# Optimization experiments

Hardware: AMD Instinct MI355X
Metric: run time of the kernel (lower is better)

## Reference

```python
import jax, jax.numpy as jnp
import numpy as np

B, C, T = 8, 256, 2048
DS = 4
SC = C // DS          # tsa_scale = 64
DEPTH = 256           # temporal_depth (band width)
BN_EPS = 1e-5


def _conv_bn_relu(x, W, b, g, beta, mu, var):
    # 1x1 conv on [B, C, T, 1] layout == channel matmul, then eval-mode BN, then ReLU
    y = jnp.einsum('bctz,oc->botz', x, W) + b[None, :, None, None]
    inv = g / jnp.sqrt(var + BN_EPS)
    y = (y - mu[None, :, None, None]) * inv[None, :, None, None] + beta[None, :, None, None]
    return jax.nn.relu(y)


def setup_inputs() -> dict:
    key = jax.random.key(0)
    ks = jax.random.split(key, 20)
    inp = {"x": jax.random.normal(ks[0], (B, C, T, 1), jnp.float32)}
    for name, oc, base in (("k", SC, 1), ("q", SC, 7), ("v", C, 13)):
        inp[name + "W"] = jax.random.normal(ks[base], (oc, C), jnp.float32) * 0.05
        inp[name + "b"] = jax.random.normal(ks[base + 1], (oc,), jnp.float32) * 0.05
        inp[name + "g"] = 1.0 + 0.05 * jax.random.normal(ks[base + 2], (oc,), jnp.float32)
        inp[name + "beta"] = jax.random.normal(ks[base + 3], (oc,), jnp.float32) * 0.05
        inp[name + "mu"] = jax.random.normal(ks[base + 4], (oc,), jnp.float32) * 0.05
        inp[name + "var"] = 1.0 + 0.1 * jax.random.uniform(ks[base + 5], (oc,), jnp.float32)
    return inp


def reference(x, kW, kb, kg, kbeta, kmu, kvar,
              qW, qb, qg, qbeta, qmu, qvar,
              vW, vb, vg, vbeta, vmu, vvar):
    key = _conv_bn_relu(x, kW, kb, kg, kbeta, kmu, kvar)[..., 0]                      # [B, SC, T]
    query = _conv_bn_relu(x, qW, qb, qg, qbeta, qmu, qvar)[..., 0].transpose(0, 2, 1)  # [B, T, SC]
    value = _conv_bn_relu(x, vW, vb, vg, vbeta, vmu, vvar)[..., 0].transpose(0, 2, 1)  # [B, T, C]

    i = jnp.arange(T)
    # tril(diag=0) * triu(diag=-(DEPTH-1)): causal band of width DEPTH
    mask = ((i[:, None] >= i[None, :]) & (i[:, None] - i[None, :] <= DEPTH - 1)).astype(x.dtype)

    s = jnp.einsum('btd,bds->bts', query, key) * mask / np.float32(np.sqrt(SC))
    s = jnp.exp(s - jnp.max(s, axis=2, keepdims=True)) * mask
    # NOTE: original torch code does `torch.sum(...)[0]`, indexing batch 0 of the
    # sum tensor ([T,1]) and broadcasting it across the batch. Replicated faithfully.
    s = s / (jnp.sum(s, axis=2, keepdims=True)[0] + 1e-30)

    tsa_out = jnp.einsum('bts,bsc->btc', s, value)                                     # [B, T, C]
    return x + tsa_out.transpose(0, 2, 1)[..., None]                                   # res_skip
```

## Files before the change

### kernel.cpp

```cpp
#include <hip/hip_runtime.h>

#define TDIM 2048

typedef __bf16 bf16_t;
typedef bf16_t bf16x8 __attribute__((ext_vector_type(8)));
typedef float f32x4 __attribute__((ext_vector_type(4)));
typedef unsigned short us8 __attribute__((ext_vector_type(8)));

__device__ __forceinline__ unsigned short f2bf(float x) {
  unsigned u = __builtin_bit_cast(unsigned, x);
  u += 0x7fffu + ((u >> 16) & 1u);
  return (unsigned short)(u >> 16);
}

__device__ __forceinline__ void gl_lds16(const unsigned short* g, unsigned short* l) {
  __builtin_amdgcn_global_load_lds(
      (const __attribute__((address_space(1))) unsigned int*)g,
      (__attribute__((address_space(3))) unsigned int*)l, 16, 0, 0);
}

__global__ __launch_bounds__(256) void k_prepw(
    const float* __restrict__ kW, const float* __restrict__ kb,
    const float* __restrict__ kg, const float* __restrict__ kbe,
    const float* __restrict__ kmu, const float* __restrict__ kva,
    const float* __restrict__ qW, const float* __restrict__ qb,
    const float* __restrict__ qg, const float* __restrict__ qbe,
    const float* __restrict__ qmu, const float* __restrict__ qva,
    const float* __restrict__ vW, const float* __restrict__ vb,
    const float* __restrict__ vg, const float* __restrict__ vbe,
    const float* __restrict__ vmu, const float* __restrict__ vva,
    unsigned short* __restrict__ effWf,
    float* __restrict__ effb)
{
  const int idx = blockIdx.x;
  const int tid = threadIdx.x;
  const int gid = idx >> 2, cc = idx & 3;
  unsigned short* dst = effWf + (size_t)idx * 8192;
#pragma unroll
  for (int pass = 0; pass < 4; ++pass) {
    int f = pass * 256 + tid;
    int ocblk = f >> 7, cblk = (f >> 4) & 7, m = f & 15;
    int G = gid * 128 + ocblk * 16 + m;
    const float* Wp = (G < 64) ? (kW + G * 256)
                     : (G < 128) ? (qW + (G - 64) * 256)
                                 : (vW + (G - 128) * 256);
    float gg = (G < 64) ? kg[G]  : (G < 128) ? qg[G - 64]  : vg[G - 128];
    float vr = (G < 64) ? kva[G] : (G < 128) ? qva[G - 64] : vva[G - 128];
    float inv = gg * rsqrtf(vr + 1e-5f);
    int c = cc * 64 + cblk * 8;
    float4 a = *(const float4*)(Wp + c);
    float4 bq = *(const float4*)(Wp + c + 4);
    ushort4 lo, hi;
    lo.x = f2bf(a.x * inv);  lo.y = f2bf(a.y * inv);
    lo.z = f2bf(a.z * inv);  lo.w = f2bf(a.w * inv);
    hi.x = f2bf(bq.x * inv); hi.y = f2bf(bq.y * inv);
    hi.z = f2bf(bq.z * inv); hi.w = f2bf(bq.w * inv);
    *(ushort4*)(dst + f * 8) = lo;
    *(ushort4*)(dst + f * 8 + 4) = hi;
  }
  if (idx == 0) {
    for (int G = tid; G < 384; G += 256) {
      float gg = (G < 64) ? kg[G]  : (G < 128) ? qg[G - 64]  : vg[G - 128];
      float vr = (G < 64) ? kva[G] : (G < 128) ? qva[G - 64] : vva[G - 128];
      float bb = (G < 64) ? kb[G]  : (G < 128) ? qb[G - 64]  : vb[G - 128];
      float mm = (G < 64) ? kmu[G] : (G < 128) ? qmu[G - 64] : vmu[G - 128];
      float be = (G < 64) ? kbe[G] : (G < 128) ? qbe[G - 64] : vbe[G - 128];
      float inv = gg * rsqrtf(vr + 1e-5f);
      effb[G] = (bb - mm) * inv + be;
    }
  }
}

__global__ __launch_bounds__(256, 3) void k_qkv(
    const unsigned short* __restrict__ effWf,
    const float* __restrict__ effb,
    const float* __restrict__ x,
    unsigned short* __restrict__ vv,
    unsigned short* __restrict__ kTs,
    unsigned short* __restrict__ qTs)
{
  const int tb = blockIdx.x, gid = blockIdx.y, b = blockIdx.z;
  const int tid = threadIdx.x;
  const int lane = tid & 63, wv = tid >> 6;
  const int m = lane & 15, quad = lane >> 4;
  const int t0 = tb * 64;

  __shared__ unsigned short Wb[2][8192];
  __shared__ unsigned short Xs[4608];
  __shared__ float effbs[128];

  if (tid < 128) effbs[tid] = effb[gid * 128 + tid];

  const unsigned short* wbase = effWf + (size_t)gid * 32768;
  const float* xb = x + (size_t)b * 256 * TDIM + t0 + lane;

  float xr[16];

  auto stageW = [&](int cc, int bufi) {
    const unsigned short* ws = wbase + cc * 8192;
#pragma unroll
    for (int i = 0; i < 4; ++i) {
      int ii = wv * 4 + i;
      gl_lds16(ws + (ii * 64 + lane) * 8, &Wb[bufi][ii * 512]);
    }
  };
  auto loadX = [&](int cc) {
#pragma unroll
    for (int p = 0; p < 4; ++p)
#pragma unroll
      for (int j = 0; j < 4; ++j) {
        int c = cc * 64 + p * 16 + wv * 4 + j;
        xr[p * 4 + j] = xb[(size_t)c * TDIM];
      }
  };

  const f32x4 fz = {0.f, 0.f, 0.f, 0.f};
  f32x4 acc[2][4];
#pragma unroll
  for (int i = 0; i < 2; ++i)
#pragma unroll
    for (int j = 0; j < 4; ++j) acc[i][j] = fz;

  stageW(0, 0);
  loadX(0);
  for (int cc = 0; cc < 4; ++cc) {
    __syncthreads();
#pragma unroll
    for (int p = 0; p < 4; ++p) {
      int cb4 = p * 16 + wv * 4;
      int swz = (((cb4 >> 3) ^ (lane >> 3)) << 3) | (cb4 & 7);
      ushort4 s4;
      s4.x = f2bf(xr[p * 4 + 0]); s4.y = f2bf(xr[p * 4 + 1]);
      s4.z = f2bf(xr[p * 4 + 2]); s4.w = f2bf(xr[p * 4 + 3]);
      *(ushort4*)&Xs[lane * 72 + swz] = s4;
    }
    if (cc < 3) { stageW(cc + 1, (cc + 1) & 1); loadX(cc + 1); }
    __syncthreads();
    const unsigned short* Wc = Wb[cc & 1];
#pragma unroll
    for (int kk = 0; kk < 2; ++kk) {
      int cb = kk * 4 + quad;
      bf16x8 af[2], bfv[4];
#pragma unroll
      for (int mt = 0; mt < 2; ++mt)
        af[mt] = *(const bf16x8*)&Wc[(((wv * 2 + mt) * 8 + cb) * 16 + m) * 8];
#pragma unroll
      for (int nt = 0; nt < 4; ++nt) {
        int t = nt * 16 + m;
        bfv[nt] = *(const bf16x8*)&Xs[t * 72 + ((cb ^ (t >> 3)) << 3)];
      }
#pragma unroll
      for (int mt = 0; mt < 2; ++mt)
#pragma unroll
        for (int nt = 0; nt < 4; ++nt)
          acc[mt][nt] = __builtin_amdgcn_mfma_f32_16x16x32_bf16(af[mt], bfv[nt], acc[mt][nt], 0, 0, 0);
    }
  }

  if (gid == 0) {
#pragma unroll
    for (int mt = 0; mt < 2; ++mt)
#pragma unroll
      for (int nt = 0; nt < 4; ++nt) {
        int ocl = wv * 32 + mt * 16 + quad * 4;
        int t = t0 + nt * 16 + m;
        ushort4 s4;
        s4.x = f2bf(fmaxf(acc[mt][nt][0] + effbs[ocl + 0], 0.f));
        s4.y = f2bf(fmaxf(acc[mt][nt][1] + effbs[ocl + 1], 0.f));
        s4.z = f2bf(fmaxf(acc[mt][nt][2] + effbs[ocl + 2], 0.f));
        s4.w = f2bf(fmaxf(acc[mt][nt][3] + effbs[ocl + 3], 0.f));
        if (ocl < 64) {
          int col = (((ocl >> 3) ^ (t & 7)) << 3) | (ocl & 7);
          *(ushort4*)(kTs + ((size_t)(b * TDIM + t)) * 64 + col) = s4;
        } else {
          int oq = ocl - 64;
          int col = (((oq >> 3) ^ (t & 7)) << 3) | (oq & 7);
          *(ushort4*)(qTs + ((size_t)(b * TDIM + t)) * 64 + col) = s4;
        }
      }
  } else {
#pragma unroll
    for (int mt = 0; mt < 2; ++mt)
#pragma unroll
      for (int nt = 0; nt < 4; ++nt)
#pragma unroll
        for (int r = 0; r < 4; ++r) {
          int ocl = wv * 32 + mt * 16 + quad * 4 + r;
          float y = fmaxf(acc[mt][nt][r] + effbs[ocl], 0.f);
          int c = (gid - 1) * 128 + ocl;
          int t = t0 + nt * 16 + m;
          vv[(size_t)(b * 256 + c) * TDIM + t] = f2bf(y);
        }
  }
}

__global__ __launch_bounds__(512, 1) void k_denom(
    const unsigned short* __restrict__ kTs,
    const unsigned short* __restrict__ qTs,
    float* __restrict__ denom0)
{
  const int t0d = blockIdx.x * 16;
  const int tid = threadIdx.x;
  const int lane = tid & 63, w = tid >> 6;
  const int m = lane & 15, quad = lane >> 4;

  __shared__ unsigned short S[18432];
  unsigned short* Qs = S;
  unsigned short* Ks = S + 1024;
  __shared__ float pmaxs[8][16];
  __shared__ float psums[8][16];

  {
    const unsigned short* qg = qTs + (size_t)t0d * 64;
    const unsigned short* kg = kTs + ((long)t0d - 256) * 64;
#pragma unroll
    for (int it = 0; it < 5; ++it) {
      int j = it * 512 + tid;
      if (j < 2304) {
        const unsigned short* g = (j < 128) ? (qg + j * 8) : (kg + (size_t)(j - 128) * 8);
        gl_lds16(g, &S[(it * 512 + w * 64) * 8]);
      }
    }
  }
  __syncthreads();

  const int jn = (w == 0) ? 3 : 2;
  f32x4 sc[3];
  {
    int t = m;
    bf16x8 qf0 = *(const bf16x8*)&Qs[t * 64 + ((quad ^ (t & 7)) << 3)];
    bf16x8 qf1 = *(const bf16x8*)&Qs[t * 64 + (((4 + quad) ^ (t & 7)) << 3)];
    const f32x4 fz = {0.f, 0.f, 0.f, 0.f};
#pragma unroll
    for (int jj = 0; jj < 3; ++jj) {
      if (jj < jn) {
        int j = w + jj * 8;
        int sr = 16 * j + m;
        f32x4 a = fz;
        bf16x8 kf0 = *(const bf16x8*)&Ks[sr * 64 + ((quad ^ (sr & 7)) << 3)];
        a = __builtin_amdgcn_mfma_f32_16x16x32_bf16(qf0, kf0, a, 0, 0, 0);
        bf16x8 kf1 = *(const bf16x8*)&Ks[sr * 64 + (((4 + quad) ^ (sr & 7)) << 3)];
        a = __builtin_amdgcn_mfma_f32_16x16x32_bf16(qf1, kf1, a, 0, 0, 0);
        sc[jj] = a;
      }
    }
  }

  float mx[4] = {0.f, 0.f, 0.f, 0.f};
#pragma unroll
  for (int jj = 0; jj < 3; ++jj)
    if (jj < jn) {
      int j = w + jj * 8;
#pragma unroll
      for (int r = 0; r < 4; ++r) {
        float v = sc[jj][r] * 0.125f;
        sc[jj][r] = v;
        int tg = t0d + quad * 4 + r;
        int sg = t0d - 256 + 16 * j + m;
        if (sg >= 0 && sg <= tg && tg - sg < 256) mx[r] = fmaxf(mx[r], v);
      }
    }
#pragma unroll
  for (int d = 1; d < 16; d <<= 1)
#pragma unroll
    for (int r = 0; r < 4; ++r) mx[r] = fmaxf(mx[r], __shfl_xor(mx[r], d, 64));
  if (m == 0)
#pragma unroll
    for (int r = 0; r < 4; ++r) pmaxs[w][quad * 4 + r] = mx[r];
  __syncthreads();

  float mxf[4];
#pragma unroll
  for (int r = 0; r < 4; ++r) {
    float v = pmaxs[0][quad * 4 + r];
#pragma unroll
    for (int ww = 1; ww < 8; ++ww) v = fmaxf(v, pmaxs[ww][quad * 4 + r]);
    mxf[r] = v;
  }
  float sm[4] = {0.f, 0.f, 0.f, 0.f};
#pragma unroll
  for (int jj = 0; jj < 3; ++jj)
    if (jj < jn) {
      int j = w + jj * 8;
#pragma unroll
      for (int r = 0; r < 4; ++r) {
        int tg = t0d + quad * 4 + r;
        int sg = t0d - 256 + 16 * j + m;
        if (sg >= 0 && sg <= tg && tg - sg < 256) sm[r] += __expf(sc[jj][r] - mxf[r]);
      }
    }
#pragma unroll
  for (int d = 1; d < 16; d <<= 1)
#pragma unroll
    for (int r = 0; r < 4; ++r) sm[r] += __shfl_xor(sm[r], d, 64);
  if (m == 0)
#pragma unroll
    for (int r = 0; r < 4; ++r) psums[w][quad * 4 + r] = sm[r];
  __syncthreads();

  if (tid < 16) {
    float s = 0.f;
#pragma unroll
    for (int ww = 0; ww < 8; ++ww) s += psums[ww][tid];
    denom0[t0d + tid] = s;
  }
}

__global__ __launch_bounds__(512, 4) void k_attn(
    const float* __restrict__ x,
    const unsigned short* __restrict__ vv,
    const unsigned short* __restrict__ kTs,
    const unsigned short* __restrict__ qTs,
    const float* __restrict__ denom0,
    float* __restrict__ out)
{
  const int tb = blockIdx.x, ch = blockIdx.y, b = blockIdx.z;
  const int tid = threadIdx.x;
  const int lane = tid & 63, w = tid >> 6;
  const int m = lane & 15, quad = lane >> 4;
  const int t0 = tb * 64;

  __shared__ unsigned short SM[24576];
  __shared__ float pmaxs[128];
  unsigned short* Qs = SM;
  unsigned short* Ks = SM + 4096;
  unsigned short* Ps = SM;

  {
    const unsigned short* qg = qTs + ((size_t)(b * TDIM + t0)) * 64;
    const unsigned short* kg = kTs + ((long)(b * TDIM + t0) - 256) * 64;
#pragma unroll
    for (int it = 0; it < 6; ++it) {
      int j = it * 512 + tid;
      const unsigned short* g = (j < 512) ? (qg + (size_t)j * 8)
                                          : (kg + (size_t)(j - 512) * 8);
      gl_lds16(g, &SM[(it * 512 + w * 64) * 8]);
    }
  }
  const int rt = w & 3, half = w >> 2;
  const int tw = t0 + rt * 16;
  float dval[4];
#pragma unroll
  for (int r = 0; r < 4; ++r) dval[r] = denom0[tw + quad * 4 + r];
  __syncthreads();

  const int j0 = half ? 9 : 0;
  const int jn = half ? 8 : 9;
  f32x4 sc[9];
  {
    int t = rt * 16 + m;
    bf16x8 qf0 = *(const bf16x8*)&Qs[t * 64 + ((quad ^ (t & 7)) << 3)];
    bf16x8 qf1 = *(const bf16x8*)&Qs[t * 64 + (((4 + quad) ^ (t & 7)) << 3)];
    const f32x4 fz = {0.f, 0.f, 0.f, 0.f};
#pragma unroll
    for (int jj = 0; jj < 9; ++jj) {
      if (jj < jn) {
        int sr = 16 * (rt + j0 + jj) + m;
        f32x4 a = fz;
        bf16x8 kf0 = *(const bf16x8*)&Ks[sr * 64 + ((quad ^ (sr & 7)) << 3)];
        a = __builtin_amdgcn_mfma_f32_16x16x32_bf16(qf0, kf0, a, 0, 0, 0);
        bf16x8 kf1 = *(const bf16x8*)&Ks[sr * 64 + (((4 + quad) ^ (sr & 7)) << 3)];
        a = __builtin_amdgcn_mfma_f32_16x16x32_bf16(qf1, kf1, a, 0, 0, 0);
        sc[jj] = a;
      }
    }
  }

  float mx[4] = {0.f, 0.f, 0.f, 0.f};
#pragma unroll
  for (int jj = 0; jj < 9; ++jj)
    if (jj < jn) {
#pragma unroll
      for (int r = 0; r < 4; ++r) {
        float v = sc[jj][r] * 0.125f;
        sc[jj][r] = v;
        int tg = tw + quad * 4 + r;
        int sg = t0 - 256 + 16 * (rt + j0 + jj) + m;
        if (sg >= 0 && sg <= tg && tg - sg < 256) mx[r] = fmaxf(mx[r], v);
      }
    }
#pragma unroll
  for (int d = 1; d < 16; d <<= 1)
#pragma unroll
    for (int r = 0; r < 4; ++r) mx[r] = fmaxf(mx[r], __shfl_xor(mx[r], d, 64));
  if (m == 0)
#pragma unroll
    for (int r = 0; r < 4; ++r) pmaxs[half * 64 + rt * 16 + quad * 4 + r] = mx[r];

  __syncthreads();

  float mxf[4], rden[4];
#pragma unroll
  for (int r = 0; r < 4; ++r) {
    int row = rt * 16 + quad * 4 + r;
    mxf[r] = fmaxf(pmaxs[row], pmaxs[64 + row]);
    rden[r] = 1.f / (dval[r] + 1e-30f);
  }
#pragma unroll
  for (int jj = 0; jj < 9; ++jj)
    if (jj < jn) {
#pragma unroll
      for (int r = 0; r < 4; ++r) {
        int tg = tw + quad * 4 + r;
        int sg = t0 - 256 + 16 * (rt + j0 + jj) + m;
        bool ib = (sg >= 0 && sg <= tg && tg - sg < 256);
        sc[jj][r] = ib ? __expf(sc[jj][r] - mxf[r]) * rden[r] : 0.f;
      }
    }

  if (half == 0) {
    if (rt > 0) {
      int row = rt * 16 + (lane >> 2), col = 16 * rt - 16 + (lane & 3) * 4;
      ushort4 z; z.x = 0; z.y = 0; z.z = 0; z.w = 0;
      *(ushort4*)&Ps[row * 344 + col] = z;
    }
  } else {
    if (rt < 3) {
      int row = rt * 16 + (lane >> 2), col = 16 * rt + 272 + (lane & 3) * 4;
      ushort4 z; z.x = 0; z.y = 0; z.z = 0; z.w = 0;
      *(ushort4*)&Ps[row * 344 + col] = z;
    }
  }
#pragma unroll
  for (int jj = 0; jj < 9; ++jj)
    if (jj < jn) {
      int col = 16 * (rt + j0 + jj) + m;
#pragma unroll
      for (int r = 0; r < 4; ++r)
        Ps[(rt * 16 + quad * 4 + r) * 344 + col] = f2bf(sc[jj][r]);
    }

  const int cbase = ch * 128 + w * 16;
  const unsigned short* vrow = vv + (size_t)(b * 256 + cbase + m) * TDIM;
  us8 vreg = {0, 0, 0, 0, 0, 0, 0, 0};
  if (t0 >= 256) vreg = *(const us8*)(vrow + t0 - 256 + quad * 8);

  __syncthreads();

  const f32x4 fz = {0.f, 0.f, 0.f, 0.f};
  f32x4 acc[4] = {fz, fz, fz, fz};
#pragma unroll
  for (int chunk = 0; chunk < 10; ++chunk) {
    us8 vnext = {0, 0, 0, 0, 0, 0, 0, 0};
    if (chunk < 9) {
      int sbase = t0 - 256 + (chunk + 1) * 32;
      if (sbase >= 0) vnext = *(const us8*)(vrow + sbase + quad * 8);
    }
    bf16x8 bfr = __builtin_bit_cast(bf16x8, vreg);
#pragma unroll
    for (int mt = 0; mt < 4; ++mt) {
      const int cs = mt >> 1;
      if (chunk >= cs && chunk <= cs + 8) {
        bf16x8 af = *(const bf16x8*)&Ps[(mt * 16 + m) * 344 + chunk * 32 + quad * 8];
        acc[mt] = __builtin_amdgcn_mfma_f32_16x16x32_bf16(af, bfr, acc[mt], 0, 0, 0);
      }
    }
    vreg = vnext;
  }

#pragma unroll
  for (int mt = 0; mt < 4; ++mt) {
    int c = cbase + m;
    int t = t0 + mt * 16 + quad * 4;
    size_t off = (size_t)(b * 256 + c) * TDIM + t;
    float4 xv = *(const float4*)(x + off);
    float4 o;
    o.x = xv.x + acc[mt][0];
    o.y = xv.y + acc[mt][1];
    o.z = xv.z + acc[mt][2];
    o.w = xv.w + acc[mt][3];
    *(float4*)(out + off) = o;
  }
}

extern "C" void kernel_launch(void* const* d_in, const int* in_sizes, int n_in,
                              void* d_out, int out_size, void* d_ws, size_t ws_size,
                              hipStream_t stream) {
  const float* x   = (const float*)d_in[0];
  const float* kW  = (const float*)d_in[1];
  const float* kb  = (const float*)d_in[2];
  const float* kg  = (const float*)d_in[3];
  const float* kbe = (const float*)d_in[4];
  const float* kmu = (const float*)d_in[5];
  const float* kva = (const float*)d_in[6];
  const float* qW  = (const float*)d_in[7];
  const float* qb  = (const float*)d_in[8];
  const float* qg  = (const float*)d_in[9];
  const float* qbe = (const float*)d_in[10];
  const float* qmu = (const float*)d_in[11];
  const float* qva = (const float*)d_in[12];
  const float* vW  = (const float*)d_in[13];
  const float* vb  = (const float*)d_in[14];
  const float* vg  = (const float*)d_in[15];
  const float* vbe = (const float*)d_in[16];
  const float* vmu = (const float*)d_in[17];
  const float* vva = (const float*)d_in[18];

  unsigned short* vv  = (unsigned short*)d_ws;
  unsigned short* kTs = vv + (size_t)8 * 256 * TDIM;
  unsigned short* qTs = kTs + (size_t)8 * TDIM * 64;
  float* denom0 = (float*)(qTs + (size_t)8 * TDIM * 64);
  unsigned short* effWf = (unsigned short*)(denom0 + 2048);
  float* effb = (float*)(effWf + 12 * 8192);
  float* outp = (float*)d_out;

  k_prepw<<<dim3(12), 256, 0, stream>>>(
      kW, kb, kg, kbe, kmu, kva,
      qW, qb, qg, qbe, qmu, qva,
      vW, vb, vg, vbe, vmu, vva, effWf, effb);
  k_qkv<<<dim3(32, 3, 8), 256, 0, stream>>>(effWf, effb, x, vv, kTs, qTs);
  k_denom<<<dim3(128), 512, 0, stream>>>(kTs, qTs, denom0);
  k_attn<<<dim3(32, 2, 8), 512, 0, stream>>>(x, vv, kTs, qTs, denom0, outp);
}
```

Baseline: 133.7 us.

## Compute all 256 channels per attention block to avoid recomputing scores

Each k_attn block now covers all 256 value channels (two 16-channel tiles per wave) instead of splitting channels across two blocks. The QK^T score and softmax work per time tile is therefore done once rather than twice. Block indices are swizzled so adjacent blocks take spread-out time tiles, and the residual x loads are issued before the MFMA loop. In exchange the grid is halved to 256 blocks, register use rises (launch bounds occupancy hint lowered from 4 to 2), and per-block latency grows.

```diff
diff --git a/kernel.cpp b/kernel.cpp
--- a/kernel.cpp
+++ b/kernel.cpp
@@ -306,7 +306,7 @@
   }
 }
 
-__global__ __launch_bounds__(512, 4) void k_attn(
+__global__ __launch_bounds__(512, 2) void k_attn(
     const float* __restrict__ x,
     const unsigned short* __restrict__ vv,
     const unsigned short* __restrict__ kTs,
@@ -314,7 +314,8 @@
     const float* __restrict__ denom0,
     float* __restrict__ out)
 {
-  const int tb = blockIdx.x, ch = blockIdx.y, b = blockIdx.z;
+  const int bx = blockIdx.x, b = blockIdx.y;
+  const int tb = (bx >> 3) + 4 * (bx & 7);
   const int tid = threadIdx.x;
   const int lane = tid & 63, w = tid >> 6;
   const int m = lane & 15, quad = lane >> 4;
@@ -430,47 +431,69 @@
         Ps[(rt * 16 + quad * 4 + r) * 344 + col] = f2bf(sc[jj][r]);
     }
 
-  const int cbase = ch * 128 + w * 16;
-  const unsigned short* vrow = vv + (size_t)(b * 256 + cbase + m) * TDIM;
-  us8 vreg = {0, 0, 0, 0, 0, 0, 0, 0};
-  if (t0 >= 256) vreg = *(const us8*)(vrow + t0 - 256 + quad * 8);
+  const int cbase = w * 32;
+  const unsigned short* vrow0 = vv + (size_t)(b * 256 + cbase + m) * TDIM;
+  const unsigned short* vrow1 = vrow0 + (size_t)16 * TDIM;
+  us8 vreg0 = {0, 0, 0, 0, 0, 0, 0, 0}, vreg1 = {0, 0, 0, 0, 0, 0, 0, 0};
+  if (t0 >= 256) {
+    vreg0 = *(const us8*)(vrow0 + t0 - 256 + quad * 8);
+    vreg1 = *(const us8*)(vrow1 + t0 - 256 + quad * 8);
+  }
 
   __syncthreads();
 
+  float4 xv[4][2];
+#pragma unroll
+  for (int mt = 0; mt < 4; ++mt)
+#pragma unroll
+    for (int ct = 0; ct < 2; ++ct) {
+      int c = cbase + ct * 16 + m;
+      int t = t0 + mt * 16 + quad * 4;
+      xv[mt][ct] = *(const float4*)(x + (size_t)(b * 256 + c) * TDIM + t);
+    }
+
   const f32x4 fz = {0.f, 0.f, 0.f, 0.f};
-  f32x4 acc[4] = {fz, fz, fz, fz};
+  f32x4 acc[4][2];
+#pragma unroll
+  for (int i = 0; i < 4; ++i) { acc[i][0] = fz; acc[i][1] = fz; }
 #pragma unroll
   for (int chunk = 0; chunk < 10; ++chunk) {
-    us8 vnext = {0, 0, 0, 0, 0, 0, 0, 0};
+    us8 vn0 = {0, 0, 0, 0, 0, 0, 0, 0}, vn1 = {0, 0, 0, 0, 0, 0, 0, 0};
     if (chunk < 9) {
       int sbase = t0 - 256 + (chunk + 1) * 32;
-      if (sbase >= 0) vnext = *(const us8*)(vrow + sbase + quad * 8);
-    }
-    bf16x8 bfr = __builtin_bit_cast(bf16x8, vreg);
+      if (sbase >= 0) {
+        vn0 = *(const us8*)(vrow0 + sbase + quad * 8);
+        vn1 = *(const us8*)(vrow1 + sbase + quad * 8);
+      }
+    }
+    bf16x8 bfr0 = __builtin_bit_cast(bf16x8, vreg0);
+    bf16x8 bfr1 = __builtin_bit_cast(bf16x8, vreg1);
 #pragma unroll
     for (int mt = 0; mt < 4; ++mt) {
       const int cs = mt >> 1;
       if (chunk >= cs && chunk <= cs + 8) {
         bf16x8 af = *(const bf16x8*)&Ps[(mt * 16 + m) * 344 + chunk * 32 + quad * 8];
-        acc[mt] = __builtin_amdgcn_mfma_f32_16x16x32_bf16(af, bfr, acc[mt], 0, 0, 0);
-      }
-    }
-    vreg = vnext;
-  }
-
-#pragma unroll
-  for (int mt = 0; mt < 4; ++mt) {
-    int c = cbase + m;
-    int t = t0 + mt * 16 + quad * 4;
-    size_t off = (size_t)(b * 256 + c) * TDIM + t;
-    float4 xv = *(const float4*)(x + off);
-    float4 o;
-    o.x = xv.x + acc[mt][0];
-    o.y = xv.y + acc[mt][1];
-    o.z = xv.z + acc[mt][2];
-    o.w = xv.w + acc[mt][3];
-    *(float4*)(out + off) = o;
-  }
+        acc[mt][0] = __builtin_amdgcn_mfma_f32_16x16x32_bf16(af, bfr0, acc[mt][0], 0, 0, 0);
+        acc[mt][1] = __builtin_amdgcn_mfma_f32_16x16x32_bf16(af, bfr1, acc[mt][1], 0, 0, 0);
+      }
+    }
+    vreg0 = vn0; vreg1 = vn1;
+  }
+
+#pragma unroll
+  for (int mt = 0; mt < 4; ++mt)
+#pragma unroll
+    for (int ct = 0; ct < 2; ++ct) {
+      int c = cbase + ct * 16 + m;
+      int t = t0 + mt * 16 + quad * 4;
+      size_t off = (size_t)(b * 256 + c) * TDIM + t;
+      float4 o;
+      o.x = xv[mt][ct].x + acc[mt][ct][0];
+      o.y = xv[mt][ct].y + acc[mt][ct][1];
+      o.z = xv[mt][ct].z + acc[mt][ct][2];
+      o.w = xv[mt][ct].w + acc[mt][ct][3];
+      *(float4*)(out + off) = o;
+    }
 }
 
 extern "C" void kernel_launch(void* const* d_in, const int* in_sizes, int n_in,
@@ -510,5 +533,5 @@
       vW, vb, vg, vbe, vmu, vva, effWf, effb);
   k_qkv<<<dim3(32, 3, 8), 256, 0, stream>>>(effWf, effb, x, vv, kTs, qTs);
   k_denom<<<dim3(128), 512, 0, stream>>>(kTs, qTs, denom0);
-  k_attn<<<dim3(32, 2, 8), 512, 0, stream>>>(x, vv, kTs, qTs, denom0, outp);
-}
+  k_attn<<<dim3(32, 8), 512, 0, stream>>>(x, vv, kTs, qTs, denom0, outp);
+}
```

After: 132.3 us (median of 2 runs). No clear change (-1.0%).

## Fuse all four kernels into one cooperative kernel with grid syncs

Applied to the files above, without the earlier changes.

Replaces the four launches (weight prep, QKV projection, batch-0 denominator, attention) with a single cooperative kernel of 256 blocks of 1024 threads, separated by three grid-wide barriers. The aim is to remove launch gaps and the separate denominator pass, since batch-0 blocks now compute the denominator from scores they already hold. Each block handles all 256 channels for its 64 time steps, so scores are computed once per tile instead of once per channel half, and the warp split of the score band changes. The cost is grid-sync overhead, 1024-thread blocks with heavier register and LDS pressure, and idle blocks during the weight-prep phase.

```diff
diff --git a/kernel.cpp b/kernel.cpp
--- a/kernel.cpp
+++ b/kernel.cpp
@@ -1,4 +1,5 @@
 #include <hip/hip_runtime.h>
+#include <hip/hip_cooperative_groups.h>
 
 #define TDIM 2048
 
@@ -19,7 +20,8 @@
       (__attribute__((address_space(3))) unsigned int*)l, 16, 0, 0);
 }
 
-__global__ __launch_bounds__(256) void k_prepw(
+__global__ __launch_bounds__(1024, 4) void k_fused(
+    const float* __restrict__ x,
     const float* __restrict__ kW, const float* __restrict__ kb,
     const float* __restrict__ kg, const float* __restrict__ kbe,
     const float* __restrict__ kmu, const float* __restrict__ kva,
@@ -29,331 +31,186 @@
     const float* __restrict__ vW, const float* __restrict__ vb,
     const float* __restrict__ vg, const float* __restrict__ vbe,
     const float* __restrict__ vmu, const float* __restrict__ vva,
-    unsigned short* __restrict__ effWf,
-    float* __restrict__ effb)
-{
-  const int idx = blockIdx.x;
-  const int tid = threadIdx.x;
-  const int gid = idx >> 2, cc = idx & 3;
-  unsigned short* dst = effWf + (size_t)idx * 8192;
-#pragma unroll
-  for (int pass = 0; pass < 4; ++pass) {
-    int f = pass * 256 + tid;
-    int ocblk = f >> 7, cblk = (f >> 4) & 7, m = f & 15;
-    int G = gid * 128 + ocblk * 16 + m;
-    const float* Wp = (G < 64) ? (kW + G * 256)
-                     : (G < 128) ? (qW + (G - 64) * 256)
-                                 : (vW + (G - 128) * 256);
-    float gg = (G < 64) ? kg[G]  : (G < 128) ? qg[G - 64]  : vg[G - 128];
-    float vr = (G < 64) ? kva[G] : (G < 128) ? qva[G - 64] : vva[G - 128];
-    float inv = gg * rsqrtf(vr + 1e-5f);
-    int c = cc * 64 + cblk * 8;
-    float4 a = *(const float4*)(Wp + c);
-    float4 bq = *(const float4*)(Wp + c + 4);
-    ushort4 lo, hi;
-    lo.x = f2bf(a.x * inv);  lo.y = f2bf(a.y * inv);
-    lo.z = f2bf(a.z * inv);  lo.w = f2bf(a.w * inv);
-    hi.x = f2bf(bq.x * inv); hi.y = f2bf(bq.y * inv);
-    hi.z = f2bf(bq.z * inv); hi.w = f2bf(bq.w * inv);
-    *(ushort4*)(dst + f * 8) = lo;
-    *(ushort4*)(dst + f * 8 + 4) = hi;
-  }
-  if (idx == 0) {
-    for (int G = tid; G < 384; G += 256) {
-      float gg = (G < 64) ? kg[G]  : (G < 128) ? qg[G - 64]  : vg[G - 128];
-      float vr = (G < 64) ? kva[G] : (G < 128) ? qva[G - 64] : vva[G - 128];
-      float bb = (G < 64) ? kb[G]  : (G < 128) ? qb[G - 64]  : vb[G - 128];
-      float mm = (G < 64) ? kmu[G] : (G < 128) ? qmu[G - 64] : vmu[G - 128];
-      float be = (G < 64) ? kbe[G] : (G < 128) ? qbe[G - 64] : vbe[G - 128];
-      float inv = gg * rsqrtf(vr + 1e-5f);
-      effb[G] = (bb - mm) * inv + be;
-    }
-  }
-}
-
-__global__ __launch_bounds__(256, 3) void k_qkv(
-    const unsigned short* __restrict__ effWf,
-    const float* __restrict__ effb,
-    const float* __restrict__ x,
     unsigned short* __restrict__ vv,
     unsigned short* __restrict__ kTs,
-    unsigned short* __restrict__ qTs)
+    unsigned short* __restrict__ qTs,
+    float* __restrict__ denom0,
+    unsigned short* __restrict__ effWf,
+    float* __restrict__ effb,
+    float* __restrict__ out)
 {
-  const int tb = blockIdx.x, gid = blockIdx.y, b = blockIdx.z;
-  const int tid = threadIdx.x;
-  const int lane = tid & 63, wv = tid >> 6;
-  const int m = lane & 15, quad = lane >> 4;
-  const int t0 = tb * 64;
-
-  __shared__ unsigned short Wb[2][8192];
-  __shared__ unsigned short Xs[4608];
-  __shared__ float effbs[128];
-
-  if (tid < 128) effbs[tid] = effb[gid * 128 + tid];
-
-  const unsigned short* wbase = effWf + (size_t)gid * 32768;
-  const float* xb = x + (size_t)b * 256 * TDIM + t0 + lane;
-
-  float xr[16];
-
-  auto stageW = [&](int cc, int bufi) {
-    const unsigned short* ws = wbase + cc * 8192;
-#pragma unroll
-    for (int i = 0; i < 4; ++i) {
-      int ii = wv * 4 + i;
-      gl_lds16(ws + (ii * 64 + lane) * 8, &Wb[bufi][ii * 512]);
-    }
-  };
-  auto loadX = [&](int cc) {
-#pragma unroll
-    for (int p = 0; p < 4; ++p)
-#pragma unroll
-      for (int j = 0; j < 4; ++j) {
-        int c = cc * 64 + p * 16 + wv * 4 + j;
-        xr[p * 4 + j] = xb[(size_t)c * TDIM];
-      }
-  };
-
-  const f32x4 fz = {0.f, 0.f, 0.f, 0.f};
-  f32x4 acc[2][4];
-#pragma unroll
-  for (int i = 0; i < 2; ++i)
-#pragma unroll
-    for (int j = 0; j < 4; ++j) acc[i][j] = fz;
-
-  stageW(0, 0);
-  loadX(0);
-  for (int cc = 0; cc < 4; ++cc) {
-    __syncthreads();
-#pragma unroll
-    for (int p = 0; p < 4; ++p) {
-      int cb4 = p * 16 + wv * 4;
-      int swz = (((cb4 >> 3) ^ (lane >> 3)) << 3) | (cb4 & 7);
-      ushort4 s4;
-      s4.x = f2bf(xr[p * 4 + 0]); s4.y = f2bf(xr[p * 4 + 1]);
-      s4.z = f2bf(xr[p * 4 + 2]); s4.w = f2bf(xr[p * 4 + 3]);
-      *(ushort4*)&Xs[lane * 72 + swz] = s4;
-    }
-    if (cc < 3) { stageW(cc + 1, (cc + 1) & 1); loadX(cc + 1); }
-    __syncthreads();
-    const unsigned short* Wc = Wb[cc & 1];
-#pragma unroll
-    for (int kk = 0; kk < 2; ++kk) {
-      int cb = kk * 4 + quad;
-      bf16x8 af[2], bfv[4];
-#pragma unroll
-      for (int mt = 0; mt < 2; ++mt)
-        af[mt] = *(const bf16x8*)&Wc[(((wv * 2 + mt) * 8 + cb) * 16 + m) * 8];
-#pragma unroll
-      for (int nt = 0; nt < 4; ++nt) {
-        int t = nt * 16 + m;
-        bfv[nt] = *(const bf16x8*)&Xs[t * 72 + ((cb ^ (t >> 3)) << 3)];
-      }
-#pragma unroll
-      for (int mt = 0; mt < 2; ++mt)
-#pragma unroll
-        for (int nt = 0; nt < 4; ++nt)
-          acc[mt][nt] = __builtin_amdgcn_mfma_f32_16x16x32_bf16(af[mt], bfv[nt], acc[mt][nt], 0, 0, 0);
-    }
-  }
-
-  if (gid == 0) {
-#pragma unroll
-    for (int mt = 0; mt < 2; ++mt)
-#pragma unroll
-      for (int nt = 0; nt < 4; ++nt) {
-        int ocl = wv * 32 + mt * 16 + quad * 4;
-        int t = t0 + nt * 16 + m;
-        ushort4 s4;
-        s4.x = f2bf(fmaxf(acc[mt][nt][0] + effbs[ocl + 0], 0.f));
-        s4.y = f2bf(fmaxf(acc[mt][nt][1] + effbs[ocl + 1], 0.f));
-        s4.z = f2bf(fmaxf(acc[mt][nt][2] + effbs[ocl + 2], 0.f));
-        s4.w = f2bf(fmaxf(acc[mt][nt][3] + effbs[ocl + 3], 0.f));
-        if (ocl < 64) {
-          int col = (((ocl >> 3) ^ (t & 7)) << 3) | (ocl & 7);
-          *(ushort4*)(kTs + ((size_t)(b * TDIM + t)) * 64 + col) = s4;
-        } else {
-          int oq = ocl - 64;
-          int col = (((oq >> 3) ^ (t & 7)) << 3) | (oq & 7);
-          *(ushort4*)(qTs + ((size_t)(b * TDIM + t)) * 64 + col) = s4;
-        }
-      }
-  } else {
-#pragma unroll
-    for (int mt = 0; mt < 2; ++mt)
-#pragma unroll
-      for (int nt = 0; nt < 4; ++nt)
-#pragma unroll
-        for (int r = 0; r < 4; ++r) {
-          int ocl = wv * 32 + mt * 16 + quad * 4 + r;
-          float y = fmaxf(acc[mt][nt][r] + effbs[ocl], 0.f);
-          int c = (gid - 1) * 128 + ocl;
-          int t = t0 + nt * 16 + m;
-          vv[(size_t)(b * 256 + c) * TDIM + t] = f2bf(y);
-        }
-  }
-}
-
-__global__ __launch_bounds__(512, 1) void k_denom(
-    const unsigned short* __restrict__ kTs,
-    const unsigned short* __restrict__ qTs,
-    float* __restrict__ denom0)
-{
-  const int t0d = blockIdx.x * 16;
+  const int tx = blockIdx.x, b = blockIdx.y;
   const int tid = threadIdx.x;
   const int lane = tid & 63, w = tid >> 6;
   const int m = lane & 15, quad = lane >> 4;
-
-  __shared__ unsigned short S[18432];
-  unsigned short* Qs = S;
-  unsigned short* Ks = S + 1024;
-  __shared__ float pmaxs[8][16];
-  __shared__ float psums[8][16];
+  const int t0 = tx * 64;
+
+  __shared__ unsigned short SM[29184];
+  __shared__ float pmaxs[256];
+  __shared__ float psums[256];
+
+  cooperative_groups::grid_group gg = cooperative_groups::this_grid();
 
   {
-    const unsigned short* qg = qTs + (size_t)t0d * 64;
-    const unsigned short* kg = kTs + ((long)t0d - 256) * 64;
-#pragma unroll
-    for (int it = 0; it < 5; ++it) {
-      int j = it * 512 + tid;
-      if (j < 2304) {
-        const unsigned short* g = (j < 128) ? (qg + j * 8) : (kg + (size_t)(j - 128) * 8);
-        gl_lds16(g, &S[(it * 512 + w * 64) * 8]);
-      }
-    }
-  }
-  __syncthreads();
-
-  const int jn = (w == 0) ? 3 : 2;
-  f32x4 sc[3];
+    int gtid = (b * 32 + tx) * 1024 + tid;
+    if (gtid < 12288) {
+      int idx = gtid >> 10, f = gtid & 1023;
+      int gid = idx >> 2, cc = idx & 3;
+      int ocblk = f >> 7, cblk = (f >> 4) & 7, mm = f & 15;
+      int G = gid * 128 + ocblk * 16 + mm;
+      const float* Wp = (G < 64) ? (kW + G * 256)
+                       : (G < 128) ? (qW + (G - 64) * 256)
+                                   : (vW + (G - 128) * 256);
+      float ggn = (G < 64) ? kg[G]  : (G < 128) ? qg[G - 64]  : vg[G - 128];
+      float vr  = (G < 64) ? kva[G] : (G < 128) ? qva[G - 64] : vva[G - 128];
+      float inv = ggn * rsqrtf(vr + 1e-5f);
+      int c = cc * 64 + cblk * 8;
+      float4 a = *(const float4*)(Wp + c);
+      float4 bq = *(const float4*)(Wp + c + 4);
+      ushort4 lo, hi;
+      lo.x = f2bf(a.x * inv);  lo.y = f2bf(a.y * inv);
+      lo.z = f2bf(a.z * inv);  lo.w = f2bf(a.w * inv);
+      hi.x = f2bf(bq.x * inv); hi.y = f2bf(bq.y * inv);
+      hi.z = f2bf(bq.z * inv); hi.w = f2bf(bq.w * inv);
+      unsigned short* dst = effWf + (size_t)idx * 8192 + f * 8;
+      *(ushort4*)dst = lo;
+      *(ushort4*)(dst + 4) = hi;
+    } else if (gtid < 12672) {
+      int G = gtid - 12288;
+      float ggn = (G < 64) ? kg[G]  : (G < 128) ? qg[G - 64]  : vg[G - 128];
+      float vr  = (G < 64) ? kva[G] : (G < 128) ? qva[G - 64] : vva[G - 128];
+      float bb  = (G < 64) ? kb[G]  : (G < 128) ? qb[G - 64]  : vb[G - 128];
+      float mm  = (G < 64) ? kmu[G] : (G < 128) ? qmu[G - 64] : vmu[G - 128];
+      float be  = (G < 64) ? kbe[G] : (G < 128) ? qbe[G - 64] : vbe[G - 128];
+      float inv = ggn * rsqrtf(vr + 1e-5f);
+      effb[G] = (bb - mm) * inv + be;
+    }
+  }
+  __threadfence();
+  gg.sync();
+
   {
-    int t = m;
-    bf16x8 qf0 = *(const bf16x8*)&Qs[t * 64 + ((quad ^ (t & 7)) << 3)];
-    bf16x8 qf1 = *(const bf16x8*)&Qs[t * 64 + (((4 + quad) ^ (t & 7)) << 3)];
+    unsigned short* Wb = SM;
+    unsigned short* Xs = SM + 24576;
+    const int ow = w & 7, th = w >> 3;
+    const int cg = tid >> 6;
+    const float* xb = x + (size_t)b * 256 * TDIM + t0 + (tid & 63);
+    float xr[4];
     const f32x4 fz = {0.f, 0.f, 0.f, 0.f};
-#pragma unroll
-    for (int jj = 0; jj < 3; ++jj) {
-      if (jj < jn) {
-        int j = w + jj * 8;
-        int sr = 16 * j + m;
-        f32x4 a = fz;
-        bf16x8 kf0 = *(const bf16x8*)&Ks[sr * 64 + ((quad ^ (sr & 7)) << 3)];
-        a = __builtin_amdgcn_mfma_f32_16x16x32_bf16(qf0, kf0, a, 0, 0, 0);
-        bf16x8 kf1 = *(const bf16x8*)&Ks[sr * 64 + (((4 + quad) ^ (sr & 7)) << 3)];
-        a = __builtin_amdgcn_mfma_f32_16x16x32_bf16(qf1, kf1, a, 0, 0, 0);
-        sc[jj] = a;
-      }
-    }
-  }
-
-  float mx[4] = {0.f, 0.f, 0.f, 0.f};
-#pragma unroll
-  for (int jj = 0; jj < 3; ++jj)
-    if (jj < jn) {
-      int j = w + jj * 8;
-#pragma unroll
-      for (int r = 0; r < 4; ++r) {
-        float v = sc[jj][r] * 0.125f;
-        sc[jj][r] = v;
-        int tg = t0d + quad * 4 + r;
-        int sg = t0d - 256 + 16 * j + m;
-        if (sg >= 0 && sg <= tg && tg - sg < 256) mx[r] = fmaxf(mx[r], v);
-      }
-    }
-#pragma unroll
-  for (int d = 1; d < 16; d <<= 1)
-#pragma unroll
-    for (int r = 0; r < 4; ++r) mx[r] = fmaxf(mx[r], __shfl_xor(mx[r], d, 64));
-  if (m == 0)
-#pragma unroll
-    for (int r = 0; r < 4; ++r) pmaxs[w][quad * 4 + r] = mx[r];
-  __syncthreads();
-
-  float mxf[4];
-#pragma unroll
-  for (int r = 0; r < 4; ++r) {
-    float v = pmaxs[0][quad * 4 + r];
-#pragma unroll
-    for (int ww = 1; ww < 8; ++ww) v = fmaxf(v, pmaxs[ww][quad * 4 + r]);
-    mxf[r] = v;
-  }
-  float sm[4] = {0.f, 0.f, 0.f, 0.f};
-#pragma unroll
-  for (int jj = 0; jj < 3; ++jj)
-    if (jj < jn) {
-      int j = w + jj * 8;
-#pragma unroll
-      for (int r = 0; r < 4; ++r) {
-        int tg = t0d + quad * 4 + r;
-        int sg = t0d - 256 + 16 * j + m;
-        if (sg >= 0 && sg <= tg && tg - sg < 256) sm[r] += __expf(sc[jj][r] - mxf[r]);
-      }
-    }
-#pragma unroll
-  for (int d = 1; d < 16; d <<= 1)
-#pragma unroll
-    for (int r = 0; r < 4; ++r) sm[r] += __shfl_xor(sm[r], d, 64);
-  if (m == 0)
-#pragma unroll
-    for (int r = 0; r < 4; ++r) psums[w][quad * 4 + r] = sm[r];
-  __syncthreads();
-
-  if (tid < 16) {
-    float s = 0.f;
-#pragma unroll
-    for (int ww = 0; ww < 8; ++ww) s += psums[ww][tid];
-    denom0[t0d + tid] = s;
-  }
-}
-
-__global__ __launch_bounds__(512, 4) void k_attn(
-    const float* __restrict__ x,
-    const unsigned short* __restrict__ vv,
-    const unsigned short* __restrict__ kTs,
-    const unsigned short* __restrict__ qTs,
-    const float* __restrict__ denom0,
-    float* __restrict__ out)
-{
-  const int tb = blockIdx.x, ch = blockIdx.y, b = blockIdx.z;
-  const int tid = threadIdx.x;
-  const int lane = tid & 63, w = tid >> 6;
-  const int m = lane & 15, quad = lane >> 4;
-  const int t0 = tb * 64;
-
-  __shared__ unsigned short SM[24576];
-  __shared__ float pmaxs[128];
+    f32x4 acc[3][2];
+#pragma unroll
+    for (int j = 0; j < 3; ++j) { acc[j][0] = fz; acc[j][1] = fz; }
+
+#pragma unroll
+    for (int j = 0; j < 4; ++j) xr[j] = xb[(size_t)(cg * 4 + j) * TDIM];
+
+    for (int cc = 0; cc < 4; ++cc) {
+      __syncthreads();
+#pragma unroll
+      for (int it = 0; it < 3; ++it) {
+        int j = it * 1024 + tid;
+        int rg = j >> 10, jj = j & 1023;
+        gl_lds16(effWf + (size_t)(rg * 4 + cc) * 8192 + jj * 8,
+                 &Wb[(it * 1024 + w * 64) * 8]);
+      }
+      {
+        int t = tid & 63;
+        int cb4 = cg * 4;
+        int swz = (((cb4 >> 3) ^ (t >> 3)) << 3) | (cb4 & 7);
+        ushort4 s4;
+        s4.x = f2bf(xr[0]); s4.y = f2bf(xr[1]);
+        s4.z = f2bf(xr[2]); s4.w = f2bf(xr[3]);
+        *(ushort4*)&Xs[t * 72 + swz] = s4;
+      }
+      if (cc < 3) {
+#pragma unroll
+        for (int j = 0; j < 4; ++j)
+          xr[j] = xb[(size_t)((cc + 1) * 64 + cg * 4 + j) * TDIM];
+      }
+      __syncthreads();
+#pragma unroll
+      for (int kk = 0; kk < 2; ++kk) {
+        int cb = kk * 4 + quad;
+        bf16x8 af[3], bfv[2];
+#pragma unroll
+        for (int j = 0; j < 3; ++j) {
+          int ob = ow * 3 + j;
+          af[j] = *(const bf16x8*)&Wb[((ob >> 3) * 1024 + ((ob & 7) * 8 + cb) * 16 + m) * 8];
+        }
+#pragma unroll
+        for (int nt = 0; nt < 2; ++nt) {
+          int t = (th * 2 + nt) * 16 + m;
+          bfv[nt] = *(const bf16x8*)&Xs[t * 72 + ((cb ^ (t >> 3)) << 3)];
+        }
+#pragma unroll
+        for (int j = 0; j < 3; ++j)
+#pragma unroll
+          for (int nt = 0; nt < 2; ++nt)
+            acc[j][nt] = __builtin_amdgcn_mfma_f32_16x16x32_bf16(af[j], bfv[nt], acc[j][nt], 0, 0, 0);
+      }
+    }
+#pragma unroll
+    for (int j = 0; j < 3; ++j) {
+      int ob = ow * 3 + j;
+      int ocb = ob * 16 + quad * 4;
+      float bia[4];
+#pragma unroll
+      for (int r = 0; r < 4; ++r) bia[r] = effb[ocb + r];
+#pragma unroll
+      for (int nt = 0; nt < 2; ++nt) {
+        int t = t0 + (th * 2 + nt) * 16 + m;
+        float y0 = fmaxf(acc[j][nt][0] + bia[0], 0.f);
+        float y1 = fmaxf(acc[j][nt][1] + bia[1], 0.f);
+        float y2 = fmaxf(acc[j][nt][2] + bia[2], 0.f);
+        float y3 = fmaxf(acc[j][nt][3] + bia[3], 0.f);
+        if (ob < 8) {
+          ushort4 s4;
+          s4.x = f2bf(y0); s4.y = f2bf(y1); s4.z = f2bf(y2); s4.w = f2bf(y3);
+          int oc6 = ocb & 63;
+          int col = (((oc6 >> 3) ^ (t & 7)) << 3) | (oc6 & 7);
+          unsigned short* dst = ((ob < 4) ? kTs : qTs) + (size_t)(b * TDIM + t) * 64 + col;
+          *(ushort4*)dst = s4;
+        } else {
+          int c = ocb - 128;
+          vv[(size_t)(b * 256 + c + 0) * TDIM + t] = f2bf(y0);
+          vv[(size_t)(b * 256 + c + 1) * TDIM + t] = f2bf(y1);
+          vv[(size_t)(b * 256 + c + 2) * TDIM + t] = f2bf(y2);
+          vv[(size_t)(b * 256 + c + 3) * TDIM + t] = f2bf(y3);
+        }
+      }
+    }
+  }
+  __threadfence();
+  gg.sync();
+
   unsigned short* Qs = SM;
   unsigned short* Ks = SM + 4096;
   unsigned short* Ps = SM;
-
   {
-    const unsigned short* qg = qTs + ((size_t)(b * TDIM + t0)) * 64;
+    const unsigned short* qg = qTs + (size_t)(b * TDIM + t0) * 64;
     const unsigned short* kg = kTs + ((long)(b * TDIM + t0) - 256) * 64;
 #pragma unroll
-    for (int it = 0; it < 6; ++it) {
-      int j = it * 512 + tid;
-      const unsigned short* g = (j < 512) ? (qg + (size_t)j * 8)
-                                          : (kg + (size_t)(j - 512) * 8);
-      gl_lds16(g, &SM[(it * 512 + w * 64) * 8]);
-    }
-  }
+    for (int it = 0; it < 3; ++it) {
+      int j = it * 1024 + tid;
+      const unsigned short* g = (j < 512) ? qg + (size_t)j * 8
+                                          : kg + (size_t)(j - 512) * 8;
+      gl_lds16(g, &SM[(it * 1024 + w * 64) * 8]);
+    }
+  }
+  __syncthreads();
+
   const int rt = w & 3, half = w >> 2;
   const int tw = t0 + rt * 16;
-  float dval[4];
-#pragma unroll
-  for (int r = 0; r < 4; ++r) dval[r] = denom0[tw + quad * 4 + r];
-  __syncthreads();
-
-  const int j0 = half ? 9 : 0;
-  const int jn = half ? 8 : 9;
-  f32x4 sc[9];
+  const int j0 = (half == 0) ? 0 : (half == 1) ? 5 : (half == 2) ? 9 : 13;
+  const int jn = (half == 0) ? 5 : 4;
+  f32x4 sc[5];
   {
     int t = rt * 16 + m;
     bf16x8 qf0 = *(const bf16x8*)&Qs[t * 64 + ((quad ^ (t & 7)) << 3)];
     bf16x8 qf1 = *(const bf16x8*)&Qs[t * 64 + (((4 + quad) ^ (t & 7)) << 3)];
     const f32x4 fz = {0.f, 0.f, 0.f, 0.f};
 #pragma unroll
-    for (int jj = 0; jj < 9; ++jj) {
+    for (int jj = 0; jj < 5; ++jj)
       if (jj < jn) {
         int sr = 16 * (rt + j0 + jj) + m;
         f32x4 a = fz;
@@ -363,12 +220,10 @@
         a = __builtin_amdgcn_mfma_f32_16x16x32_bf16(qf1, kf1, a, 0, 0, 0);
         sc[jj] = a;
       }
-    }
-  }
-
+  }
   float mx[4] = {0.f, 0.f, 0.f, 0.f};
 #pragma unroll
-  for (int jj = 0; jj < 9; ++jj)
+  for (int jj = 0; jj < 5; ++jj)
     if (jj < jn) {
 #pragma unroll
       for (int r = 0; r < 4; ++r) {
@@ -386,18 +241,47 @@
   if (m == 0)
 #pragma unroll
     for (int r = 0; r < 4; ++r) pmaxs[half * 64 + rt * 16 + quad * 4 + r] = mx[r];
-
   __syncthreads();
 
-  float mxf[4], rden[4];
+  float mxf[4];
 #pragma unroll
   for (int r = 0; r < 4; ++r) {
     int row = rt * 16 + quad * 4 + r;
-    mxf[r] = fmaxf(pmaxs[row], pmaxs[64 + row]);
-    rden[r] = 1.f / (dval[r] + 1e-30f);
-  }
-#pragma unroll
-  for (int jj = 0; jj < 9; ++jj)
+    mxf[r] = fmaxf(fmaxf(pmaxs[row], pmaxs[64 + row]),
+                   fmaxf(pmaxs[128 + row], pmaxs[192 + row]));
+  }
+  if (b == 0) {
+    float smv[4] = {0.f, 0.f, 0.f, 0.f};
+#pragma unroll
+    for (int jj = 0; jj < 5; ++jj)
+      if (jj < jn) {
+#pragma unroll
+        for (int r = 0; r < 4; ++r) {
+          int tg = tw + quad * 4 + r;
+          int sg = t0 - 256 + 16 * (rt + j0 + jj) + m;
+          if (sg >= 0 && sg <= tg && tg - sg < 256) smv[r] += __expf(sc[jj][r] - mxf[r]);
+        }
+      }
+#pragma unroll
+    for (int d = 1; d < 16; d <<= 1)
+#pragma unroll
+      for (int r = 0; r < 4; ++r) smv[r] += __shfl_xor(smv[r], d, 64);
+    if (m == 0)
+#pragma unroll
+      for (int r = 0; r < 4; ++r) psums[half * 64 + rt * 16 + quad * 4 + r] = smv[r];
+    __syncthreads();
+    if (tid < 64)
+      denom0[t0 + tid] = psums[tid] + psums[64 + tid] + psums[128 + tid] + psums[192 + tid];
+  }
+  __threadfence();
+  gg.sync();
+
+  float rden[4];
+#pragma unroll
+  for (int r = 0; r < 4; ++r)
+    rden[r] = 1.f / (denom0[tw + quad * 4 + r] + 1e-30f);
+#pragma unroll
+  for (int jj = 0; jj < 5; ++jj)
     if (jj < jn) {
 #pragma unroll
       for (int r = 0; r < 4; ++r) {
@@ -408,21 +292,18 @@
       }
     }
 
-  if (half == 0) {
-    if (rt > 0) {
-      int row = rt * 16 + (lane >> 2), col = 16 * rt - 16 + (lane & 3) * 4;
-      ushort4 z; z.x = 0; z.y = 0; z.z = 0; z.w = 0;
-      *(ushort4*)&Ps[row * 344 + col] = z;
-    }
-  } else {
-    if (rt < 3) {
-      int row = rt * 16 + (lane >> 2), col = 16 * rt + 272 + (lane & 3) * 4;
-      ushort4 z; z.x = 0; z.y = 0; z.z = 0; z.w = 0;
-      *(ushort4*)&Ps[row * 344 + col] = z;
-    }
-  }
-#pragma unroll
-  for (int jj = 0; jj < 9; ++jj)
+  if (half == 1 && rt > 0) {
+    int row = rt * 16 + (lane >> 2), col = 16 * rt - 16 + (lane & 3) * 4;
+    ushort4 z; z.x = 0; z.y = 0; z.z = 0; z.w = 0;
+    *(ushort4*)&Ps[row * 344 + col] = z;
+  }
+  if (half == 2 && rt < 3) {
+    int row = rt * 16 + (lane >> 2), col = 16 * rt + 272 + (lane & 3) * 4;
+    ushort4 z; z.x = 0; z.y = 0; z.z = 0; z.w = 0;
+    *(ushort4*)&Ps[row * 344 + col] = z;
+  }
+#pragma unroll
+  for (int jj = 0; jj < 5; ++jj)
     if (jj < jn) {
       int col = 16 * (rt + j0 + jj) + m;
 #pragma unroll
@@ -430,21 +311,28 @@
         Ps[(rt * 16 + quad * 4 + r) * 344 + col] = f2bf(sc[jj][r]);
     }
 
-  const int cbase = ch * 128 + w * 16;
-  const unsigned short* vrow = vv + (size_t)(b * 256 + cbase + m) * TDIM;
+  const unsigned short* vrow = vv + (size_t)(b * 256 + w * 16 + m) * TDIM;
   us8 vreg = {0, 0, 0, 0, 0, 0, 0, 0};
   if (t0 >= 256) vreg = *(const us8*)(vrow + t0 - 256 + quad * 8);
 
   __syncthreads();
 
-  const f32x4 fz = {0.f, 0.f, 0.f, 0.f};
-  f32x4 acc[4] = {fz, fz, fz, fz};
+  float4 xv[4];
+#pragma unroll
+  for (int mt = 0; mt < 4; ++mt) {
+    int c = w * 16 + m;
+    int t = t0 + mt * 16 + quad * 4;
+    xv[mt] = *(const float4*)(x + (size_t)(b * 256 + c) * TDIM + t);
+  }
+
+  const f32x4 fz2 = {0.f, 0.f, 0.f, 0.f};
+  f32x4 acc2[4] = {fz2, fz2, fz2, fz2};
 #pragma unroll
   for (int chunk = 0; chunk < 10; ++chunk) {
-    us8 vnext = {0, 0, 0, 0, 0, 0, 0, 0};
+    us8 vn = {0, 0, 0, 0, 0, 0, 0, 0};
     if (chunk < 9) {
       int sbase = t0 - 256 + (chunk + 1) * 32;
-      if (sbase >= 0) vnext = *(const us8*)(vrow + sbase + quad * 8);
+      if (sbase >= 0) vn = *(const us8*)(vrow + sbase + quad * 8);
     }
     bf16x8 bfr = __builtin_bit_cast(bf16x8, vreg);
 #pragma unroll
@@ -452,23 +340,22 @@
       const int cs = mt >> 1;
       if (chunk >= cs && chunk <= cs + 8) {
         bf16x8 af = *(const bf16x8*)&Ps[(mt * 16 + m) * 344 + chunk * 32 + quad * 8];
-        acc[mt] = __builtin_amdgcn_mfma_f32_16x16x32_bf16(af, bfr, acc[mt], 0, 0, 0);
-      }
-    }
-    vreg = vnext;
+        acc2[mt] = __builtin_amdgcn_mfma_f32_16x16x32_bf16(af, bfr, acc2[mt], 0, 0, 0);
+      }
+    }
+    vreg = vn;
   }
 
 #pragma unroll
   for (int mt = 0; mt < 4; ++mt) {
-    int c = cbase + m;
+    int c = w * 16 + m;
     int t = t0 + mt * 16 + quad * 4;
     size_t off = (size_t)(b * 256 + c) * TDIM + t;
-    float4 xv = *(const float4*)(x + off);
     float4 o;
-    o.x = xv.x + acc[mt][0];
-    o.y = xv.y + acc[mt][1];
-    o.z = xv.z + acc[mt][2];
-    o.w = xv.w + acc[mt][3];
+    o.x = xv[mt].x + acc2[mt][0];
+    o.y = xv[mt].y + acc2[mt][1];
+    o.z = xv[mt].z + acc2[mt][2];
+    o.w = xv[mt].w + acc2[mt][3];
     *(float4*)(out + off) = o;
   }
 }
@@ -504,11 +391,14 @@
   float* effb = (float*)(effWf + 12 * 8192);
   float* outp = (float*)d_out;
 
-  k_prepw<<<dim3(12), 256, 0, stream>>>(
-      kW, kb, kg, kbe, kmu, kva,
-      qW, qb, qg, qbe, qmu, qva,
-      vW, vb, vg, vbe, vmu, vva, effWf, effb);
-  k_qkv<<<dim3(32, 3, 8), 256, 0, stream>>>(effWf, effb, x, vv, kTs, qTs);
-  k_denom<<<dim3(128), 512, 0, stream>>>(kTs, qTs, denom0);
-  k_attn<<<dim3(32, 2, 8), 512, 0, stream>>>(x, vv, kTs, qTs, denom0, outp);
+  void* args[] = {
+    (void*)&x,
+    (void*)&kW, (void*)&kb, (void*)&kg, (void*)&kbe, (void*)&kmu, (void*)&kva,
+    (void*)&qW, (void*)&qb, (void*)&qg, (void*)&qbe, (void*)&qmu, (void*)&qva,
+    (void*)&vW, (void*)&vb, (void*)&vg, (void*)&vbe, (void*)&vmu, (void*)&vva,
+    (void*)&vv, (void*)&kTs, (void*)&qTs, (void*)&denom0,
+    (void*)&effWf, (void*)&effb, (void*)&outp
+  };
+  hipLaunchCooperativeKernel((const void*)k_fused, dim3(32, 8), dim3(1024),
+                             args, 0, stream);
 }
```

After: 463.9 us. +247.0%, slower.
